# Optimization experiments

Measured on AMD Instinct MI355X. Metric: run time of the kernel, lower is better.

## Reference

```python
import jax, jax.numpy as jnp
import numpy as np

N = 262144          # pixels (512x512 image)
F = 2               # in_features (x, y)
K = 13              # num_frequencies
H = 256             # dim_hidden
OUT = 3             # out_features (RGB)
TILES = [1, 4, 16, 64, 256]   # prod(tile_dims[i]) per layer
PE_DIM = F + 2 * F * K        # 54


def setup_inputs() -> dict:
    key = jax.random.key(0)
    ks = jax.random.split(key, 2 * len(TILES) + 3)
    inp = {"coords": jax.random.uniform(ks[0], (N, F), dtype=jnp.float32)}
    d_in = PE_DIM
    for i, t in enumerate(TILES):
        # kaiming-uniform-like scale; biases init to zero as in the module
        bound = float(np.sqrt(6.0 / d_in))
        inp[f"w{i}"] = jax.random.uniform(ks[1 + i], (t, d_in, H), dtype=jnp.float32,
                                           minval=-bound, maxval=bound)
        inp[f"b{i}"] = jnp.zeros((H,), dtype=jnp.float32)
        d_in = H
    bound = float(np.sqrt(6.0 / H))
    inp["w_last"] = jax.random.uniform(ks[-1], (OUT, H), dtype=jnp.float32,
                                        minval=-bound, maxval=bound)
    inp["b_last"] = jnp.zeros((OUT,), dtype=jnp.float32)
    return inp


def _pos_enc(coords):
    # NeRF positional encoding, concat order: coords, then for each freq i,
    # for each feature j: sin(2^i * pi * c_j), cos(2^i * pi * c_j)
    freqs = (2.0 ** jnp.arange(K, dtype=jnp.float32)) * np.pi      # [K]
    ang = coords[:, None, :] * freqs[None, :, None]                # [N, K, F]
    enc = jnp.stack([jnp.sin(ang), jnp.cos(ang)], axis=-1)         # [N, K, F, 2]
    enc = enc.reshape(coords.shape[0], 2 * K * F)
    return jnp.concatenate([coords, enc], axis=-1)                 # [N, PE_DIM]


def reference(coords, w0, b0, w1, b1, w2, b2, w3, b3, w4, b4, w_last, b_last):
    x = _pos_enc(coords)                                           # [N, 54]
    for w, b in ((w0, b0), (w1, b1), (w2, b2), (w3, b3), (w4, b4)):
        t = w.shape[0]
        x = x.reshape(t, -1, x.shape[-1])                          # [T, N/T, d_in]
        x = jnp.einsum('tnd,tdo->tno', x, w) + b                   # per-tile GEMM
        x = jnp.where(x > 0, x, 0.2 * x)                           # LeakyReLU(0.2)
    x = x.reshape(-1, H)                                           # [N, H]
    return x @ w_last.T + b_last                                   # [N, OUT]
```

## Files before the change

### kernel.cpp

```cpp
#include <hip/hip_runtime.h>
#include <stdint.h>

typedef uint32_t u32;
typedef short s16x8 __attribute__((ext_vector_type(8)));
typedef float f32x16 __attribute__((ext_vector_type(16)));
typedef u32 u32x2 __attribute__((ext_vector_type(2)));
typedef u32 u32x4 __attribute__((ext_vector_type(4)));

#define NPIX   262144
#define HD     256

#define FTHR      512
#define PXB       128
#define NBLK      (NPIX / PXB)
#define ACT_LDS   65536

#define B0_OFF  0u
#define B1_OFF  32768u
#define B2_OFF  557056u
#define B3_OFF  2654208u
#define B4_OFF  11042816u
#define BH_OFF  44597248u
#define BLOB_TOTAL 44613632u
#define F_W1 2048u
#define F_W2 34816u
#define F_W3 165888u
#define F_W4 690176u
#define F_WH 2787328u
#define F_END 2788352u

#define ACT_BYTES  131072
#define WBUF_BYTES 16384
#define FB_LDS     (ACT_BYTES + 2 * WBUF_BYTES)

__device__ __forceinline__ u32 bfpair(float a, float b) {
    u32 ua = __builtin_bit_cast(u32, a);
    u32 ub = __builtin_bit_cast(u32, b);
    ua = (ua + 0x7FFFu + ((ua >> 16) & 1u)) >> 16;
    ub = (ub + 0x7FFFu + ((ub >> 16) & 1u)) >> 16;
    return ua | (ub << 16);
}
__device__ __forceinline__ u32 act_off(int row, int colByte) {
    return (u32)((row << 9) + (colByte ^ ((row & 31) << 4)));
}
__device__ __forceinline__ u32 w_off32(int col, int kByte) {
    return (u32)((col << 6) + (kByte ^ (((col >> 1) & 3) << 4)));
}

extern "C" __global__ __launch_bounds__(256)
void loe_prepass(const float* __restrict__ w0, const float* __restrict__ w1,
                 const float* __restrict__ w2, const float* __restrict__ w3,
                 const float* __restrict__ w4, const float* __restrict__ wl,
                 char* __restrict__ ws)
{
    const u32 f = blockIdx.x * 256 + threadIdx.x;
    if (f >= F_END) return;
    float v[8];
    char* dst;
    if (f < F_W1) {
        const u32 kk = f >> 9, fb = (f >> 6) & 7, lane = f & 63;
        const u32 l31 = lane & 31, lhi = lane >> 5;
        const u32 k0 = kk * 16 + lhi * 8, col = fb * 32 + l31;
        #pragma unroll
        for (int j = 0; j < 8; ++j)
            v[j] = (k0 + j < 54) ? w0[(k0 + j) * HD + col] : 0.0f;
        dst = ws + B0_OFF + (size_t)f * 16;
    } else if (f < F_WH) {
        const float* W; size_t boff; u32 fl;
        if (f < F_W2)      { W = w1; boff = B1_OFF; fl = f - F_W1; }
        else if (f < F_W3) { W = w2; boff = B2_OFF; fl = f - F_W2; }
        else if (f < F_W4) { W = w3; boff = B3_OFF; fl = f - F_W3; }
        else               { W = w4; boff = B4_OFF; fl = f - F_W4; }
        const u32 t = fl >> 13, c = fl & 8191;
        const u32 kk = c >> 9, fb = (c >> 6) & 7, lane = c & 63;
        const u32 l31 = lane & 31, lhi = lane >> 5;
        const u32 k0 = kk * 16 + lhi * 8, col = fb * 32 + l31;
        const float* src = W + (size_t)t * 65536 + (size_t)k0 * HD + col;
        #pragma unroll
        for (int j = 0; j < 8; ++j) v[j] = src[(size_t)j * HD];
        dst = ws + boff + (size_t)fl * 16;
    } else {
        const u32 fl = f - F_WH;
        const u32 kk = fl >> 6, lane = fl & 63;
        const u32 l31 = lane & 31, lhi = lane >> 5;
        const u32 k0 = kk * 16 + lhi * 8;
        #pragma unroll
        for (int j = 0; j < 8; ++j)
            v[j] = (l31 < 3) ? wl[l31 * HD + k0 + j] : 0.0f;
        dst = ws + BH_OFF + (size_t)fl * 16;
    }
    u32x4 pk;
    pk.x = bfpair(v[0], v[1]); pk.y = bfpair(v[2], v[3]);
    pk.z = bfpair(v[4], v[5]); pk.w = bfpair(v[6], v[7]);
    *reinterpret_cast<u32x4*>(dst) = pk;
}

extern "C" __global__ __launch_bounds__(FTHR, 4)
void loe_fused_pre(const float* __restrict__ coords,
                   const float* __restrict__ b0, const float* __restrict__ b1,
                   const float* __restrict__ b2, const float* __restrict__ b3,
                   const float* __restrict__ b4, const float* __restrict__ bl,
                   const char* __restrict__ blob,
                   float* __restrict__ out)
{
    extern __shared__ char lds[];

    const int tid  = threadIdx.x;
    const int lane = tid & 63;
    const int wv   = tid >> 6;
    const int l31  = lane & 31;
    const int lhi  = lane >> 5;

    const int bid  = (int)blockIdx.x;
    const int pb   = ((bid & 7) << 8) | (bid >> 3);
    const int pix0 = pb << 7;

    const size_t fragoff = (size_t)wv * 1024 + (size_t)lane * 16;
    auto ldfrag = [&](const char* base, int chunk) -> u32x4 {
        return *reinterpret_cast<const u32x4*>(base + (size_t)chunk * 8192 + fragoff);
    };

    const char* b0p = blob + B0_OFF;
    const char* b1p = blob + B1_OFF + (size_t)(pb >> 9) * 131072;
    const char* b2p = blob + B2_OFF + (size_t)(pb >> 7) * 131072;
    const char* b3p = blob + B3_OFF + (size_t)(pb >> 5) * 131072;
    const char* b4p = blob + B4_OFF + (size_t)(pb >> 3) * 131072;
    const char* bHp = blob + BH_OFF;

    u32x4 wr0 = ldfrag(b0p, 0), wr1 = ldfrag(b0p, 1),
          wr2 = ldfrag(b0p, 2), wr3 = ldfrag(b0p, 3);

    {
        const int p = tid >> 2;
        const int h = tid & 3;
        const float2 c2 = reinterpret_cast<const float2*>(coords)[pix0 + p];
        const float cf[2] = {c2.x, c2.y};
        #pragma unroll
        for (int u = 0; u < 16; u += 2) {
            float v[2];
            #pragma unroll
            for (int q = 0; q < 2; ++q) {
                const int c = h * 16 + u + q;
                float val;
                if (c < 2) val = cf[c];
                else if (c - 2 >= 52) val = 0.0f;
                else {
                    const int e = c - 2;
                    const float a = cf[(e >> 1) & 1] * (float)(1 << (e >> 2));
                    val = (e & 1) ? cospif(a) : sinpif(a);
                }
                v[q] = val;
            }
            *reinterpret_cast<u32*>(lds + act_off(p, (h * 16 + u) * 2)) = bfpair(v[0], v[1]);
        }
    }

    f32x16 acc[4];
    const u32 swz = (u32)(l31 << 4);
    u32 abase[4];
    #pragma unroll
    for (int pt = 0; pt < 4; ++pt) abase[pt] = (u32)((pt * 32 + l31) << 9);

    auto init_acc = [&](const float* Bias) {
        #pragma unroll
        for (int q = 0; q < 4; ++q) {
            const float4 bv = *reinterpret_cast<const float4*>(Bias + wv * 32 + q * 8 + lhi * 4);
            #pragma unroll
            for (int pt = 0; pt < 4; ++pt) {
                acc[pt][q * 4 + 0] = bv.x; acc[pt][q * 4 + 1] = bv.y;
                acc[pt][q * 4 + 2] = bv.z; acc[pt][q * 4 + 3] = bv.w;
            }
        }
    };

    auto epilogue = [&]() {
        #pragma unroll
        for (int q = 0; q < 4; ++q) {
            const int oc0 = wv * 32 + q * 8 + lhi * 4;
            #pragma unroll
            for (int pt = 0; pt < 4; ++pt) {
                float x[4];
                #pragma unroll
                for (int j = 0; j < 4; ++j) {
                    const float v = acc[pt][q * 4 + j];
                    x[j] = fmaxf(v, 0.2f * v);
                }
                u32x2 wo;
                wo.x = bfpair(x[0], x[1]);
                wo.y = bfpair(x[2], x[3]);
                *reinterpret_cast<u32x2*>(lds + act_off(pt * 32 + l31, oc0 * 2)) = wo;
            }
        }
    };

    auto proc = [&](const u32x4& w, int chunk) {
        const u32 cb = (u32)(chunk * 32 + lhi * 16) ^ swz;
        s16x8 af[4];
        #pragma unroll
        for (int pt = 0; pt < 4; ++pt)
            af[pt] = *reinterpret_cast<const s16x8*>(lds + abase[pt] + cb);
        const s16x8 a = __builtin_bit_cast(s16x8, w);
        #pragma unroll
        for (int pt = 0; pt < 4; ++pt)
            acc[pt] = __builtin_amdgcn_mfma_f32_32x32x16_bf16(a, af[pt], acc[pt], 0, 0, 0);
    };

    auto run_layer = [&](int KK, const char* cur, const char* nxt, const float* Bias) {
        init_acc(Bias);
        __syncthreads();
        #pragma unroll
        for (int kk = 0; kk < KK; kk += 4) {
            proc(wr0, kk + 0); wr0 = (kk + 4 < KK) ? ldfrag(cur, kk + 4) : ldfrag(nxt, 0);
            proc(wr1, kk + 1); wr1 = (kk + 5 < KK) ? ldfrag(cur, kk + 5) : ldfrag(nxt, 1);
            proc(wr2, kk + 2); wr2 = (kk + 6 < KK) ? ldfrag(cur, kk + 6) : ldfrag(nxt, 2);
            proc(wr3, kk + 3); wr3 = (kk + 7 < KK) ? ldfrag(cur, kk + 7) : ldfrag(nxt, 3);
        }
        __syncthreads();
        epilogue();
    };

    run_layer(4,  b0p, b1p, b0);
    run_layer(16, b1p, b2p, b1);
    run_layer(16, b2p, b3p, b2);
    run_layer(16, b3p, b4p, b3);
    run_layer(16, b4p, b4p, b4);

    __syncthreads();
    if (wv < 4) {
        f32x16 a;
        #pragma unroll
        for (int r = 0; r < 16; ++r) a[r] = 0.0f;
        const u32 hrow = (u32)((wv * 32 + l31) << 9);
        #pragma unroll 4
        for (int kk = 0; kk < 16; ++kk) {
            const u32x4 wh = *reinterpret_cast<const u32x4*>(bHp + (size_t)kk * 1024 + (size_t)lane * 16);
            const u32 cb = (u32)(kk * 32 + lhi * 16) ^ swz;
            const s16x8 af = *reinterpret_cast<const s16x8*>(lds + hrow + cb);
            a = __builtin_amdgcn_mfma_f32_32x32x16_bf16(__builtin_bit_cast(s16x8, wh), af, a, 0, 0, 0);
        }
        if (lhi == 0) {
            const int p = pix0 + wv * 32 + l31;
            out[p * 3 + 0] = a[0] + bl[0];
            out[p * 3 + 1] = a[1] + bl[1];
            out[p * 3 + 2] = a[2] + bl[2];
        }
    }
}

extern "C" __global__ __launch_bounds__(512, 2)
void loe_fused_fb(const float* __restrict__ coords,
                  const float* __restrict__ w0, const float* __restrict__ b0,
                  const float* __restrict__ w1, const float* __restrict__ b1,
                  const float* __restrict__ w2, const float* __restrict__ b2,
                  const float* __restrict__ w3, const float* __restrict__ b3,
                  const float* __restrict__ w4, const float* __restrict__ b4,
                  const float* __restrict__ wl, const float* __restrict__ bl,
                  float* __restrict__ out)
{
    extern __shared__ char lds[];
    const int tid  = threadIdx.x;
    const int lane = tid & 63;
    const int wv   = tid >> 6;
    const int wr   = wv >> 2;
    const int wc   = wv & 3;
    const int l31  = lane & 31;
    const int lhi  = lane >> 5;
    const int bid  = (int)blockIdx.x;
    const int pb   = ((bid & 7) << 7) | (bid >> 3);
    const int pix0 = pb << 8;
    const int scol = tid & 255;
    const int kh   = tid >> 8;

    float st[16];
    auto load_plain = [&](const float* W, int s) {
        const float* src = W + (size_t)(s * 32 + kh * 16) * HD + scol;
        #pragma unroll
        for (int j = 0; j < 16; ++j) st[j] = src[(size_t)j * HD];
    };
    auto load_guard = [&](const float* W, int s) {
        #pragma unroll
        for (int j = 0; j < 16; ++j) {
            const int k = s * 32 + kh * 16 + j;
            st[j] = (k < 54) ? W[k * HD + scol] : 0.0f;
        }
    };
    load_guard(w0, 0);
    {
        const int p = tid >> 1;
        const int h = tid & 1;
        const float2 c2 = reinterpret_cast<const float2*>(coords)[pix0 + p];
        const float cf[2] = {c2.x, c2.y};
        #pragma unroll
        for (int u = 0; u < 32; u += 2) {
            float v[2];
            #pragma unroll
            for (int q = 0; q < 2; ++q) {
                const int c = h * 32 + u + q;
                float val;
                if (c < 2) val = cf[c];
                else if (c - 2 >= 52) val = 0.0f;
                else {
                    const int e = c - 2;
                    const float a = cf[(e >> 1) & 1] * (float)(1 << (e >> 2));
                    val = (e & 1) ? cospif(a) : sinpif(a);
                }
                v[q] = val;
            }
            *reinterpret_cast<u32*>(lds + act_off(p, (h * 32 + u) * 2)) = bfpair(v[0], v[1]);
        }
    }
    f32x16 acc[4][2];
    int g = 0;
    auto epilogue = [&](const float* Bias) {
        #pragma unroll
        for (int ct = 0; ct < 2; ++ct)
            #pragma unroll
            for (int q = 0; q < 4; ++q) {
                const int oc0 = wc * 64 + ct * 32 + q * 8 + lhi * 4;
                const float4 bv = *reinterpret_cast<const float4*>(Bias + oc0);
                const float bj[4] = {bv.x, bv.y, bv.z, bv.w};
                #pragma unroll
                for (int pt = 0; pt < 4; ++pt) {
                    const int p = wr * 128 + pt * 32 + l31;
                    float x[4];
                    #pragma unroll
                    for (int j = 0; j < 4; ++j) {
                        float v = acc[pt][ct][q * 4 + j] + bj[j];
                        x[j] = (v > 0.0f) ? v : 0.2f * v;
                    }
                    u32x2 wv2;
                    wv2.x = bfpair(x[0], x[1]);
                    wv2.y = bfpair(x[2], x[3]);
                    *reinterpret_cast<u32x2*>(lds + act_off(p, oc0 * 2)) = wv2;
                }
            }
    };
    auto run_layer = [&](int S, const float* Wcur, const float* Wnext,
                         const float* Bias, bool guard) {
        #pragma unroll
        for (int pt = 0; pt < 4; ++pt)
            #pragma unroll
            for (int ct = 0; ct < 2; ++ct)
                #pragma unroll
                for (int r = 0; r < 16; ++r) acc[pt][ct][r] = 0.0f;
        for (int s = 0; s < S; ++s) {
            char* wbw = lds + ACT_BYTES + ((g & 1) ? WBUF_BYTES : 0);
            u32x4 pk0, pk1;
            pk0.x = bfpair(st[0], st[1]);   pk0.y = bfpair(st[2], st[3]);
            pk0.z = bfpair(st[4], st[5]);   pk0.w = bfpair(st[6], st[7]);
            pk1.x = bfpair(st[8], st[9]);   pk1.y = bfpair(st[10], st[11]);
            pk1.z = bfpair(st[12], st[13]); pk1.w = bfpair(st[14], st[15]);
            *reinterpret_cast<u32x4*>(wbw + w_off32(scol, kh * 32))      = pk0;
            *reinterpret_cast<u32x4*>(wbw + w_off32(scol, kh * 32 + 16)) = pk1;
            if (s + 1 < S) { if (guard) load_guard(Wcur, s + 1); else load_plain(Wcur, s + 1); }
            else if (Wnext) load_plain(Wnext, 0);
            __syncthreads();
            #pragma unroll
            for (int kt = 0; kt < 2; ++kt) {
                const int kb = kt * 32 + lhi * 16;
                s16x8 wf[2], af[4];
                #pragma unroll
                for (int ct = 0; ct < 2; ++ct)
                    wf[ct] = *reinterpret_cast<const s16x8*>(wbw + w_off32(wc * 64 + ct * 32 + l31, kb));
                #pragma unroll
                for (int pt = 0; pt < 4; ++pt)
                    af[pt] = *reinterpret_cast<const s16x8*>(lds + act_off(wr * 128 + pt * 32 + l31, s * 64 + kb));
                #pragma unroll
                for (int pt = 0; pt < 4; ++pt)
                    #pragma unroll
                    for (int ct = 0; ct < 2; ++ct)
                        acc[pt][ct] = __builtin_amdgcn_mfma_f32_32x32x16_bf16(wf[ct], af[pt], acc[pt][ct], 0, 0, 0);
            }
            ++g;
            __syncthreads();
        }
        epilogue(Bias);
        __syncthreads();
    };
    const float* w1t = w1 + (size_t)(pb >> 8) * 65536;
    const float* w2t = w2 + (size_t)(pb >> 6) * 65536;
    const float* w3t = w3 + (size_t)(pb >> 4) * 65536;
    const float* w4t = w4 + (size_t)(pb >> 2) * 65536;
    __syncthreads();
    run_layer(2, w0,  w1t, b0, true);
    run_layer(8, w1t, w2t, b1, false);
    run_layer(8, w2t, w3t, b2, false);
    run_layer(8, w3t, w4t, b3, false);
    run_layer(8, w4t, nullptr, b4, false);
    char* hw = lds + ACT_BYTES;
    #pragma unroll
    for (int rep = 0; rep < 2; ++rep) {
        const int task = rep * 512 + tid;
        const int col  = task & 31;
        const int kg   = task >> 5;
        float v[8];
        #pragma unroll
        for (int j = 0; j < 8; ++j)
            v[j] = (col < 3) ? wl[col * HD + kg * 8 + j] : 0.0f;
        u32x4 pk;
        pk.x = bfpair(v[0], v[1]); pk.y = bfpair(v[2], v[3]);
        pk.z = bfpair(v[4], v[5]); pk.w = bfpair(v[6], v[7]);
        *reinterpret_cast<u32x4*>(hw + col * 512 + ((kg * 16) ^ ((col & 7) << 4))) = pk;
    }
    __syncthreads();
    {
        f32x16 a;
        #pragma unroll
        for (int r = 0; r < 16; ++r) a[r] = 0.0f;
        #pragma unroll
        for (int kt = 0; kt < 16; ++kt) {
            const int kb = kt * 32 + lhi * 16;
            s16x8 wf = *reinterpret_cast<const s16x8*>(hw + l31 * 512 + (kb ^ ((l31 & 7) << 4)));
            s16x8 af = *reinterpret_cast<const s16x8*>(lds + act_off(wv * 32 + l31, kb));
            a = __builtin_amdgcn_mfma_f32_32x32x16_bf16(wf, af, a, 0, 0, 0);
        }
        if (lhi == 0) {
            const int p = pix0 + wv * 32 + l31;
            out[p * 3 + 0] = a[0] + bl[0];
            out[p * 3 + 1] = a[1] + bl[1];
            out[p * 3 + 2] = a[2] + bl[2];
        }
    }
}

extern "C" void kernel_launch(void* const* d_in, const int* in_sizes, int n_in,
                              void* d_out, int out_size, void* d_ws, size_t ws_size,
                              hipStream_t stream) {
    (void)in_sizes; (void)n_in; (void)out_size;
    const float* coords = (const float*)d_in[0];
    const float* w0 = (const float*)d_in[1];  const float* b0 = (const float*)d_in[2];
    const float* w1 = (const float*)d_in[3];  const float* b1 = (const float*)d_in[4];
    const float* w2 = (const float*)d_in[5];  const float* b2 = (const float*)d_in[6];
    const float* w3 = (const float*)d_in[7];  const float* b3 = (const float*)d_in[8];
    const float* w4 = (const float*)d_in[9];  const float* b4 = (const float*)d_in[10];
    const float* wl = (const float*)d_in[11]; const float* bl = (const float*)d_in[12];
    float* out = (float*)d_out;

    if (ws_size >= (size_t)BLOB_TOTAL) {
        (void)hipFuncSetAttribute((const void*)loe_fused_pre,
                                  hipFuncAttributeMaxDynamicSharedMemorySize, ACT_LDS);
        loe_prepass<<<dim3((F_END + 255) / 256), dim3(256), 0, stream>>>(
            w0, w1, w2, w3, w4, wl, (char*)d_ws);
        loe_fused_pre<<<dim3(NBLK), dim3(FTHR), ACT_LDS, stream>>>(
            coords, b0, b1, b2, b3, b4, bl, (const char*)d_ws, out);
    } else {
        (void)hipFuncSetAttribute((const void*)loe_fused_fb,
                                  hipFuncAttributeMaxDynamicSharedMemorySize, FB_LDS);
        loe_fused_fb<<<dim3(NPIX / 256), dim3(512), FB_LDS, stream>>>(
            coords, w0, b0, w1, b1, w2, b2, w3, b3, w4, b4, wl, bl, out);
    }
}
```

Baseline: 182.0 us.

## Split warp tiles 2x2 across features and pixels to halve LDS activation reads

Each of the 8 waves now covers 64 output features by 64 pixels instead of 32 features by 128 pixels. Each wave issues two global weight-fragment loads per k-chunk and two LDS activation reads instead of four. This halves LDS traffic per MFMA and doubles global weight traffic per wave. The weight prefetch depth drops from four chunks to two pairs, which could expose more global-load latency.

```diff
diff --git a/kernel.cpp b/kernel.cpp
--- a/kernel.cpp
+++ b/kernel.cpp
@@ -95,6 +95,8 @@
     *reinterpret_cast<u32x4*>(dst) = pk;
 }
 
+struct wpair { u32x4 a, b; };
+
 extern "C" __global__ __launch_bounds__(FTHR, 4)
 void loe_fused_pre(const float* __restrict__ coords,
                    const float* __restrict__ b0, const float* __restrict__ b1,
@@ -108,6 +110,8 @@
     const int tid  = threadIdx.x;
     const int lane = tid & 63;
     const int wv   = tid >> 6;
+    const int fg   = wv & 3;
+    const int pxg  = wv >> 2;
     const int l31  = lane & 31;
     const int lhi  = lane >> 5;
 
@@ -115,9 +119,13 @@
     const int pb   = ((bid & 7) << 8) | (bid >> 3);
     const int pix0 = pb << 7;
 
-    const size_t fragoff = (size_t)wv * 1024 + (size_t)lane * 16;
-    auto ldfrag = [&](const char* base, int chunk) -> u32x4 {
-        return *reinterpret_cast<const u32x4*>(base + (size_t)chunk * 8192 + fragoff);
+    const size_t frag0 = (size_t)(fg * 2 + 0) * 1024 + (size_t)lane * 16;
+    const size_t frag1 = (size_t)(fg * 2 + 1) * 1024 + (size_t)lane * 16;
+    auto ldpair = [&](const char* base, int chunk) -> wpair {
+        wpair r;
+        r.a = *reinterpret_cast<const u32x4*>(base + (size_t)chunk * 8192 + frag0);
+        r.b = *reinterpret_cast<const u32x4*>(base + (size_t)chunk * 8192 + frag1);
+        return r;
     };
 
     const char* b0p = blob + B0_OFF;
@@ -127,8 +135,7 @@
     const char* b4p = blob + B4_OFF + (size_t)(pb >> 3) * 131072;
     const char* bHp = blob + BH_OFF;
 
-    u32x4 wr0 = ldfrag(b0p, 0), wr1 = ldfrag(b0p, 1),
-          wr2 = ldfrag(b0p, 2), wr3 = ldfrag(b0p, 3);
+    wpair wr0 = ldpair(b0p, 0), wr1 = ldpair(b0p, 1);
 
     {
         const int p = tid >> 2;
@@ -155,65 +162,71 @@
         }
     }
 
-    f32x16 acc[4];
+    f32x16 acc[2][2];
     const u32 swz = (u32)(l31 << 4);
-    u32 abase[4];
+    u32 abase[2];
     #pragma unroll
-    for (int pt = 0; pt < 4; ++pt) abase[pt] = (u32)((pt * 32 + l31) << 9);
+    for (int pt = 0; pt < 2; ++pt) abase[pt] = (u32)((pxg * 64 + pt * 32 + l31) << 9);
 
     auto init_acc = [&](const float* Bias) {
         #pragma unroll
-        for (int q = 0; q < 4; ++q) {
-            const float4 bv = *reinterpret_cast<const float4*>(Bias + wv * 32 + q * 8 + lhi * 4);
-            #pragma unroll
-            for (int pt = 0; pt < 4; ++pt) {
-                acc[pt][q * 4 + 0] = bv.x; acc[pt][q * 4 + 1] = bv.y;
-                acc[pt][q * 4 + 2] = bv.z; acc[pt][q * 4 + 3] = bv.w;
-            }
-        }
+        for (int fb = 0; fb < 2; ++fb)
+            #pragma unroll
+            for (int q = 0; q < 4; ++q) {
+                const float4 bv = *reinterpret_cast<const float4*>(Bias + fg * 64 + fb * 32 + q * 8 + lhi * 4);
+                #pragma unroll
+                for (int pt = 0; pt < 2; ++pt) {
+                    acc[pt][fb][q * 4 + 0] = bv.x; acc[pt][fb][q * 4 + 1] = bv.y;
+                    acc[pt][fb][q * 4 + 2] = bv.z; acc[pt][fb][q * 4 + 3] = bv.w;
+                }
+            }
     };
 
     auto epilogue = [&]() {
         #pragma unroll
-        for (int q = 0; q < 4; ++q) {
-            const int oc0 = wv * 32 + q * 8 + lhi * 4;
-            #pragma unroll
-            for (int pt = 0; pt < 4; ++pt) {
-                float x[4];
-                #pragma unroll
-                for (int j = 0; j < 4; ++j) {
-                    const float v = acc[pt][q * 4 + j];
-                    x[j] = fmaxf(v, 0.2f * v);
+        for (int fb = 0; fb < 2; ++fb)
+            #pragma unroll
+            for (int q = 0; q < 4; ++q) {
+                const int oc0 = fg * 64 + fb * 32 + q * 8 + lhi * 4;
+                #pragma unroll
+                for (int pt = 0; pt < 2; ++pt) {
+                    float x[4];
+                    #pragma unroll
+                    for (int j = 0; j < 4; ++j) {
+                        const float v = acc[pt][fb][q * 4 + j];
+                        x[j] = fmaxf(v, 0.2f * v);
+                    }
+                    u32x2 wo;
+                    wo.x = bfpair(x[0], x[1]);
+                    wo.y = bfpair(x[2], x[3]);
+                    *reinterpret_cast<u32x2*>(lds + act_off(pxg * 64 + pt * 32 + l31, oc0 * 2)) = wo;
                 }
-                u32x2 wo;
-                wo.x = bfpair(x[0], x[1]);
-                wo.y = bfpair(x[2], x[3]);
-                *reinterpret_cast<u32x2*>(lds + act_off(pt * 32 + l31, oc0 * 2)) = wo;
-            }
-        }
-    };
-
-    auto proc = [&](const u32x4& w, int chunk) {
+            }
+    };
+
+    auto proc = [&](const wpair& w, int chunk) {
         const u32 cb = (u32)(chunk * 32 + lhi * 16) ^ swz;
-        s16x8 af[4];
-        #pragma unroll
-        for (int pt = 0; pt < 4; ++pt)
+        s16x8 af[2];
+        #pragma unroll
+        for (int pt = 0; pt < 2; ++pt)
             af[pt] = *reinterpret_cast<const s16x8*>(lds + abase[pt] + cb);
-        const s16x8 a = __builtin_bit_cast(s16x8, w);
-        #pragma unroll
-        for (int pt = 0; pt < 4; ++pt)
-            acc[pt] = __builtin_amdgcn_mfma_f32_32x32x16_bf16(a, af[pt], acc[pt], 0, 0, 0);
+        const s16x8 a0 = __builtin_bit_cast(s16x8, w.a);
+        const s16x8 a1 = __builtin_bit_cast(s16x8, w.b);
+        #pragma unroll
+        for (int pt = 0; pt < 2; ++pt)
+            acc[pt][0] = __builtin_amdgcn_mfma_f32_32x32x16_bf16(a0, af[pt], acc[pt][0], 0, 0, 0);
+        #pragma unroll
+        for (int pt = 0; pt < 2; ++pt)
+            acc[pt][1] = __builtin_amdgcn_mfma_f32_32x32x16_bf16(a1, af[pt], acc[pt][1], 0, 0, 0);
     };
 
     auto run_layer = [&](int KK, const char* cur, const char* nxt, const float* Bias) {
         init_acc(Bias);
         __syncthreads();
         #pragma unroll
-        for (int kk = 0; kk < KK; kk += 4) {
-            proc(wr0, kk + 0); wr0 = (kk + 4 < KK) ? ldfrag(cur, kk + 4) : ldfrag(nxt, 0);
-            proc(wr1, kk + 1); wr1 = (kk + 5 < KK) ? ldfrag(cur, kk + 5) : ldfrag(nxt, 1);
-            proc(wr2, kk + 2); wr2 = (kk + 6 < KK) ? ldfrag(cur, kk + 6) : ldfrag(nxt, 2);
-            proc(wr3, kk + 3); wr3 = (kk + 7 < KK) ? ldfrag(cur, kk + 7) : ldfrag(nxt, 3);
+        for (int kk = 0; kk < KK; kk += 2) {
+            proc(wr0, kk + 0); wr0 = (kk + 2 < KK) ? ldpair(cur, kk + 2) : ldpair(nxt, 0);
+            proc(wr1, kk + 1); wr1 = (kk + 3 < KK) ? ldpair(cur, kk + 3) : ldpair(nxt, 1);
         }
         __syncthreads();
         epilogue();
```

Result: slower. 199.9 us (+9.8%).
